# Kernel tuning notes

Hardware: AMD Instinct MI355X
Metric: run time of the kernel (lower is better)

Reference implementation:

```python
import jax, jax.numpy as jnp
import numpy as np

B, T = 1024, 8192


def setup_inputs() -> dict:
    key = jax.random.key(0)
    k1, k2 = jax.random.split(key)
    # phi/psi are [B, T, 2] probability-bound robustness traces in [0, 1]
    phi = jax.random.uniform(k1, (B, T, 2), dtype=jnp.float32)
    psi = jax.random.uniform(k2, (B, T, 2), dtype=jnp.float32)
    return {"phi": phi, "psi": psi}


def reference(phi, psi):
    """Until operator, interval [0, inf), exact (scale<=0) min/max.

    Original O(T^2) double loop computes, for each t:
        out[t] = max_{tau in [t, T-1]} min( min(phi[t..tau-1]), psi[tau] )
    with the empty segment (tau == t) contributing min(ones, psi[t]).
    Because min distributes over max, this satisfies the exact O(T)
    backward recurrence:
        r[t] = max( min(1, psi[t]), min(phi[t], r[t+1]) ),  r[T] = -inf
    which we evaluate with a reversed lax.scan over the time axis.
    """
    phi_t = jnp.swapaxes(phi, 0, 1)  # [T, B, 2]
    psi_t = jnp.swapaxes(psi, 0, 1)  # [T, B, 2]

    def step(carry, xs):
        p, q = xs
        v = jnp.minimum(jnp.asarray(1.0, p.dtype), q)  # tau == t term (min with ones)
        r = jnp.maximum(v, jnp.minimum(p, carry))
        return r, r

    init = jnp.full(phi_t.shape[1:], -jnp.inf, dtype=phi.dtype)  # [B, 2]
    _, out = jax.lax.scan(step, init, (phi_t, psi_t), reverse=True)
    return jnp.swapaxes(out, 0, 1)  # [B, T, 2]
```

## Files before the change

### kernel.cpp

```cpp
#include <hip/hip_runtime.h>


#define T_LEN 8192
#define NSEG  8
#define BLOCK (NSEG * 64)

__device__ __forceinline__ float rfl(float x) {
    return __int_as_float(__builtin_amdgcn_readfirstlane(__float_as_int(x)));
}

__global__ __launch_bounds__(BLOCK) void until_kernel(
    const float* __restrict__ phi, const float* __restrict__ psi,
    float* __restrict__ out)
{
    const int  row  = blockIdx.x;
    const int  tid  = threadIdx.x;
    const int  w    = tid >> 6;
    const int  lane = tid & 63;
    const float NEG = -__builtin_huge_valf();
    const float POS =  __builtin_huge_valf();

    const size_t segf4 = (size_t)row * (T_LEN / 2) + (size_t)w * 512;
    const float4* __restrict__ phi4 = (const float4*)phi + segf4;
    const float4* __restrict__ psi4 = (const float4*)psi + segf4;
    float4* __restrict__ out4 = (float4*)out + segf4;

    __shared__ alignas(16) float lds[NSEG * 1024];
    __shared__ float4 ssum[NSEG];
    float* wl = lds + w * 1024;

    float4 GAx[2], GAy[2], GBx[2], GBy[2];
    float  Sax[2], Say[2], Sbx[2], Sby[2];

#pragma unroll
    for (int r = 0; r < 2; ++r) {
#pragma unroll
        for (int kl = 0; kl < 4; ++kl) {
            const int e  = (r * 4 + kl) * 64 + lane;
            const int El = kl * 64 + lane;
            float4 P = phi4[e];
            float4 Q = psi4[e];
            float v0x = fminf(1.f, Q.x), v0y = fminf(1.f, Q.y);
            float v1x = fminf(1.f, Q.z), v1y = fminf(1.f, Q.w);
            wl[0 * 256 + El] = fmaxf(v0x, fminf(P.x, v1x));
            wl[1 * 256 + El] = fmaxf(v0y, fminf(P.y, v1y));
            wl[2 * 256 + El] = fminf(P.x, P.z);
            wl[3 * 256 + El] = fminf(P.y, P.w);
        }
        __syncthreads();
        GAx[r] = *(const float4*)(wl + 0 * 256 + lane * 4);
        GAy[r] = *(const float4*)(wl + 1 * 256 + lane * 4);
        GBx[r] = *(const float4*)(wl + 2 * 256 + lane * 4);
        GBy[r] = *(const float4*)(wl + 3 * 256 + lane * 4);
        __syncthreads();

        float hax = GAx[r].w, hay = GAy[r].w, hbx = GBx[r].w, hby = GBy[r].w;
        hax = fmaxf(GAx[r].z, fminf(GBx[r].z, hax));
        hay = fmaxf(GAy[r].z, fminf(GBy[r].z, hay));
        hbx = fminf(GBx[r].z, hbx);
        hby = fminf(GBy[r].z, hby);
        hax = fmaxf(GAx[r].y, fminf(GBx[r].y, hax));
        hay = fmaxf(GAy[r].y, fminf(GBy[r].y, hay));
        hbx = fminf(GBx[r].y, hbx);
        hby = fminf(GBy[r].y, hby);
        hax = fmaxf(GAx[r].x, fminf(GBx[r].x, hax));
        hay = fmaxf(GAy[r].x, fminf(GBy[r].x, hay));
        hbx = fminf(GBx[r].x, hbx);
        hby = fminf(GBy[r].x, hby);

#pragma unroll
        for (int off = 1; off < 64; off <<= 1) {
            float gax = __shfl_down(hax, off), gay = __shfl_down(hay, off);
            float gbx = __shfl_down(hbx, off), gby = __shfl_down(hby, off);
            bool  val = (lane + off) < 64;
            gax = val ? gax : NEG;  gay = val ? gay : NEG;
            gbx = val ? gbx : POS;  gby = val ? gby : POS;
            hax = fmaxf(hax, fminf(hbx, gax));
            hay = fmaxf(hay, fminf(hby, gay));
            hbx = fminf(hbx, gbx);
            hby = fminf(hby, gby);
        }
        Sax[r] = hax; Say[r] = hay; Sbx[r] = hbx; Sby[r] = hby;
    }

    float R0ax = rfl(Sax[0]), R0ay = rfl(Say[0]);
    float R0bx = rfl(Sbx[0]), R0by = rfl(Sby[0]);
    float R1ax = rfl(Sax[1]), R1ay = rfl(Say[1]);
    float R1bx = rfl(Sbx[1]), R1by = rfl(Sby[1]);
    if (lane == 0) {
        float wax = fmaxf(R0ax, fminf(R0bx, R1ax));
        float way = fmaxf(R0ay, fminf(R0by, R1ay));
        float wbx = fminf(R0bx, R1bx);
        float wby = fminf(R0by, R1by);
        ssum[w] = make_float4(wax, way, wbx, wby);
    }
    __syncthreads();
    float rcx = NEG, rcy = NEG;
    for (int j = NSEG - 1; j > w; --j) {
        float4 s = ssum[j];
        rcx = fmaxf(s.x, fminf(s.z, rcx));
        rcy = fmaxf(s.y, fminf(s.w, rcy));
    }

    float rinx[2], riny[2];
    rinx[1] = rcx;
    riny[1] = rcy;
    rinx[0] = fmaxf(R1ax, fminf(R1bx, rcx));
    riny[0] = fmaxf(R1ay, fminf(R1by, rcy));

#pragma unroll
    for (int r = 0; r < 2; ++r) {
        float yx = fmaxf(Sax[r], fminf(Sbx[r], rinx[r]));
        float yy = fmaxf(Say[r], fminf(Sby[r], riny[r]));
        float cx = __shfl_down(yx, 1), cy = __shfl_down(yy, 1);
        if (lane == 63) { cx = rinx[r]; cy = riny[r]; }
        float4 CX, CY;
        CX.w = cx;
        CY.w = cy;
        CX.z = fmaxf(GAx[r].w, fminf(GBx[r].w, CX.w));
        CY.z = fmaxf(GAy[r].w, fminf(GBy[r].w, CY.w));
        CX.y = fmaxf(GAx[r].z, fminf(GBx[r].z, CX.z));
        CY.y = fmaxf(GAy[r].z, fminf(GBy[r].z, CY.z));
        CX.x = fmaxf(GAx[r].y, fminf(GBx[r].y, CX.y));
        CY.x = fmaxf(GAy[r].y, fminf(GBy[r].y, CY.y));
        *(float4*)(wl +       r * 256 + lane * 4) = CX;
        *(float4*)(wl + 512 + r * 256 + lane * 4) = CY;
    }
    __syncthreads();

#pragma unroll
    for (int k = 0; k < 8; ++k) {
        const int e = k * 64 + lane;
        float4 P = phi4[e];
        float4 Q = psi4[e];
        float cx = wl[e];
        float cy = wl[512 + e];
        float r1x = fmaxf(fminf(1.f, Q.z), fminf(P.z, cx));
        float r1y = fmaxf(fminf(1.f, Q.w), fminf(P.w, cy));
        float r0x = fmaxf(fminf(1.f, Q.x), fminf(P.x, r1x));
        float r0y = fmaxf(fminf(1.f, Q.y), fminf(P.y, r1y));
        out4[e] = make_float4(r0x, r0y, r1x, r1y);
    }
}

extern "C" void kernel_launch(void* const* d_in, const int* in_sizes, int n_in,
                              void* d_out, int out_size, void* d_ws, size_t ws_size,
                              hipStream_t stream) {
    const float* phi = (const float*)d_in[0];
    const float* psi = (const float*)d_in[1];
    float* out = (float*)d_out;
    const int Bn = in_sizes[0] / (T_LEN * 2);
    until_kernel<<<Bn, BLOCK, 0, stream>>>(phi, psi, out);
}
```

Before: 181.6 us.

## Prefetch all row inputs up front and use wave-local barriers instead of block syncs

All eight phi/psi float4 loads per lane are now issued before any LDS work, so more global loads are in flight at once. Both halves of the segment are staged in a per-wave LDS region that is twice as large. The block-wide __syncthreads around the transposes are replaced by wave-level barriers, since each wave only touches its own LDS slice. A min-blocks hint of 4 is added to launch bounds. The costs are higher register use and double the LDS per block, which may lower occupancy.

```diff
diff --git a/kernel.cpp b/kernel.cpp
--- a/kernel.cpp
+++ b/kernel.cpp
@@ -9,7 +9,13 @@
     return __int_as_float(__builtin_amdgcn_readfirstlane(__float_as_int(x)));
 }
 
-__global__ __launch_bounds__(BLOCK) void until_kernel(
+__device__ __forceinline__ void wave_lds_fence() {
+    __asm__ volatile("" ::: "memory");
+    __builtin_amdgcn_wave_barrier();
+    __asm__ volatile("" ::: "memory");
+}
+
+__global__ __launch_bounds__(BLOCK, 4) void until_kernel(
     const float* __restrict__ phi, const float* __restrict__ psi,
     float* __restrict__ out)
 {
@@ -25,34 +31,40 @@
     const float4* __restrict__ psi4 = (const float4*)psi + segf4;
     float4* __restrict__ out4 = (float4*)out + segf4;
 
-    __shared__ alignas(16) float lds[NSEG * 1024];
+    __shared__ alignas(16) float lds[NSEG * 2048];
     __shared__ float4 ssum[NSEG];
-    float* wl = lds + w * 1024;
+    float* wl = lds + w * 2048;
+
+    float4 P[8], Q[8];
+#pragma unroll
+    for (int k = 0; k < 8; ++k) {
+        P[k] = phi4[k * 64 + lane];
+        Q[k] = psi4[k * 64 + lane];
+    }
+
+#pragma unroll
+    for (int k = 0; k < 8; ++k) {
+        const int r  = k >> 2;
+        const int kl = k & 3;
+        float* base = wl + r * 1024 + kl * 64 + lane;
+        float v0x = fminf(1.f, Q[k].x), v0y = fminf(1.f, Q[k].y);
+        float v1x = fminf(1.f, Q[k].z), v1y = fminf(1.f, Q[k].w);
+        base[0]   = fmaxf(v0x, fminf(P[k].x, v1x));
+        base[256] = fmaxf(v0y, fminf(P[k].y, v1y));
+        base[512] = fminf(P[k].x, P[k].z);
+        base[768] = fminf(P[k].y, P[k].w);
+    }
+    wave_lds_fence();
 
     float4 GAx[2], GAy[2], GBx[2], GBy[2];
     float  Sax[2], Say[2], Sbx[2], Sby[2];
-
 #pragma unroll
     for (int r = 0; r < 2; ++r) {
-#pragma unroll
-        for (int kl = 0; kl < 4; ++kl) {
-            const int e  = (r * 4 + kl) * 64 + lane;
-            const int El = kl * 64 + lane;
-            float4 P = phi4[e];
-            float4 Q = psi4[e];
-            float v0x = fminf(1.f, Q.x), v0y = fminf(1.f, Q.y);
-            float v1x = fminf(1.f, Q.z), v1y = fminf(1.f, Q.w);
-            wl[0 * 256 + El] = fmaxf(v0x, fminf(P.x, v1x));
-            wl[1 * 256 + El] = fmaxf(v0y, fminf(P.y, v1y));
-            wl[2 * 256 + El] = fminf(P.x, P.z);
-            wl[3 * 256 + El] = fminf(P.y, P.w);
-        }
-        __syncthreads();
-        GAx[r] = *(const float4*)(wl + 0 * 256 + lane * 4);
-        GAy[r] = *(const float4*)(wl + 1 * 256 + lane * 4);
-        GBx[r] = *(const float4*)(wl + 2 * 256 + lane * 4);
-        GBy[r] = *(const float4*)(wl + 3 * 256 + lane * 4);
-        __syncthreads();
+        const float* rb = wl + r * 1024;
+        GAx[r] = *(const float4*)(rb + 0 * 256 + lane * 4);
+        GAy[r] = *(const float4*)(rb + 1 * 256 + lane * 4);
+        GBx[r] = *(const float4*)(rb + 2 * 256 + lane * 4);
+        GBy[r] = *(const float4*)(rb + 3 * 256 + lane * 4);
 
         float hax = GAx[r].w, hay = GAy[r].w, hbx = GBx[r].w, hby = GBy[r].w;
         hax = fmaxf(GAx[r].z, fminf(GBx[r].z, hax));
@@ -126,19 +138,19 @@
         *(float4*)(wl +       r * 256 + lane * 4) = CX;
         *(float4*)(wl + 512 + r * 256 + lane * 4) = CY;
     }
-    __syncthreads();
+    wave_lds_fence();
 
 #pragma unroll
     for (int k = 0; k < 8; ++k) {
         const int e = k * 64 + lane;
-        float4 P = phi4[e];
-        float4 Q = psi4[e];
+        float4 P2 = phi4[e];
+        float4 Q2 = psi4[e];
         float cx = wl[e];
         float cy = wl[512 + e];
-        float r1x = fmaxf(fminf(1.f, Q.z), fminf(P.z, cx));
-        float r1y = fmaxf(fminf(1.f, Q.w), fminf(P.w, cy));
-        float r0x = fmaxf(fminf(1.f, Q.x), fminf(P.x, r1x));
-        float r0y = fmaxf(fminf(1.f, Q.y), fminf(P.y, r1y));
+        float r1x = fmaxf(fminf(1.f, Q2.z), fminf(P2.z, cx));
+        float r1y = fmaxf(fminf(1.f, Q2.w), fminf(P2.w, cy));
+        float r0x = fmaxf(fminf(1.f, Q2.x), fminf(P2.x, r1x));
+        float r0y = fmaxf(fminf(1.f, Q2.y), fminf(P2.y, r1y));
         out4[e] = make_float4(r0x, r0y, r1x, r1y);
     }
 }
```

Result: no change. 180.3 us (-0.7%).
